# Optimization experiments

Hardware: AMD Instinct MI355X
Metric: run time of the kernel (lower is better)

Reference implementation:

```python
import jax, jax.numpy as jnp
import numpy as np

NEG = -1e9  # max-semiring 'zero' / structural mask value


def _cky_max(pot, lengths):
    """Max-plus CKY inside pass (torch_struct CKY_CRF with MaxSemiring).

    pot: [B, N, N] label-maxed span potentials, pot[b, i, j] = score of span (i, j).
    Returns [B] best binary-tree score for each sequence of given length.
    betaA[b, i, w]      = best score of span starting at i with width w (span [i, i+w]).
    betaB[b, j, N-1-w]  = best score of span ending at j with width w.
    """
    B, N, _ = pot.shape
    term = jnp.diagonal(pot, axis1=1, axis2=2)  # [B, N] width-0 spans
    betaA = jnp.full((B, N, N), NEG, dtype=pot.dtype).at[:, :, 0].set(term)
    betaB = jnp.full((B, N, N), NEG, dtype=pot.dtype).at[:, :, N - 1].set(term)
    for w in range(1, N):
        Y = betaA[:, : N - w, :w]       # [B, N-w, w] left children, widths 0..w-1
        Z = betaB[:, w:, N - w:]        # [B, N-w, w] right children (matching splits)
        span = jnp.diagonal(pot, offset=w, axis1=1, axis2=2)  # [B, N-w] pot[b, i, i+w]
        new = jnp.max(Y + Z, axis=-1) + span
        betaA = betaA.at[:, : N - w, w].set(new)
        betaB = betaB.at[:, w:, N - w - 1].set(new)
    final = betaA[:, 0, :]  # [B, N]: final[b, l-1] = best tree over [0, l-1]
    return final[jnp.arange(B), lengths - 1]


def setup_inputs() -> dict:
    key = jax.random.key(0)
    k1, k2 = jax.random.split(key)
    B, N, L = 64, 128, 32
    logits = jax.random.normal(k1, (B, N, N, L), dtype=jnp.float32)
    labels = jax.random.randint(k2, (B, N, N), 0, L, dtype=jnp.int64)
    return {"logits": logits, "labels": labels}


def reference(logits, labels):
    B, N, _, L = logits.shape
    gold_event = jax.nn.one_hot(jnp.maximum(labels, 0), L, dtype=logits.dtype)
    logits = logits - logits[..., :1]
    lengths = jnp.sum(labels[:, 0, :] != -100, axis=-1)
    augment = 1.0 - gold_event
    # force_root_constituent=True: forbid non-constituent root span
    augment = augment.at[jnp.arange(B), 0, lengths - 1, 0].add(-1e9)
    pot = jnp.max(logits + augment, axis=-1)  # max-semiring sum over label dim
    pred_score = _cky_max(pot, lengths)                      # [B]
    gold_score = jnp.sum(logits * gold_event, axis=(1, 2, 3))  # [B]
    margin_losses = jax.nn.relu(pred_score - gold_score)
    return jnp.mean(margin_losses)
```

## Files before the change

kernel.cpp:

```cpp
#include <hip/hip_runtime.h>

#define BATCH 64
#define SEQ   128
#define NLAB  32
#define NEGF  -3.0e38f

__global__ __launch_bounds__(64) void len_kernel(
    const int* __restrict__ labels, int* __restrict__ lenbuf,
    float* __restrict__ gold)
{
    const int b = blockIdx.x;
    const int t = threadIdx.x;
    const size_t base = (size_t)b * SEQ * SEQ;
    int cnt = (labels[base + t] != -100) + (labels[base + 64 + t] != -100);
    #pragma unroll
    for (int d = 32; d; d >>= 1) cnt += __shfl_down(cnt, d, 64);
    if (t == 0) { lenbuf[b] = cnt; gold[b] = 0.0f; }
}

__global__ __launch_bounds__(256) void pot_gold_kernel(
    const float* __restrict__ logits, const int* __restrict__ labels,
    const int* __restrict__ lenbuf,
    float* __restrict__ pot, float* __restrict__ gold)
{
    const int tid = threadIdx.x;
    const int wave = tid >> 6, lane = tid & 63;
    __shared__ __align__(16) float LP[4 * 16 * 36];
    float* W = LP + wave * (16 * 36);

    const int block_cell0 = blockIdx.x * 256;
    const int b = block_cell0 >> 14;
    const int len = lenbuf[b];
    float gacc = 0.0f;

    const int wave_cell0 = block_cell0 + wave * 64;

    #pragma unroll
    for (int chunk = 0; chunk < 4; ++chunk) {
        const int c0 = wave_cell0 + chunk * 16;
        const float4* src = reinterpret_cast<const float4*>(logits) + ((size_t)c0 << 3);
        const float4 f0 = src[lane];
        const float4 f1 = src[lane + 64];
        const int lv = (lane < 16) ? labels[c0 + lane] : 0;

        {
            const int cA = lane >> 3, tA = lane & 7;
            *reinterpret_cast<float4*>(W + cA * 36 + tA * 4) = f0;
            const int q1 = lane + 64;
            const int cB = q1 >> 3, tB = q1 & 7;
            *reinterpret_cast<float4*>(W + cB * 36 + tB * 4) = f1;
        }
        const int c = lane >> 2, u = lane & 3;
        const float4 r0 = *reinterpret_cast<const float4*>(W + c * 36 + u * 8);
        const float4 r1 = *reinterpret_cast<const float4*>(W + c * 36 + u * 8 + 4);

        int lab = __shfl(lv, c, 64);
        if (lab < 0) lab = 0;
        const float l0 = __shfl(r0.x, c << 2, 64);

        const int cell = c0 + c;
        const int ci = (cell >> 7) & (SEQ - 1);
        const int cj = cell & (SEQ - 1);
        const bool special = (ci == 0) && (cj == len - 1);

        const float vv[8] = { r0.x, r0.y, r0.z, r0.w, r1.x, r1.y, r1.z, r1.w };
        float m = NEGF, g = 0.0f;
        #pragma unroll
        for (int e = 0; e < 8; ++e) {
            const int l = u * 8 + e;
            const float r = vv[e] - l0;
            const bool isg = (l == lab);
            g = isg ? r : g;
            float cand = r + (isg ? 0.0f : 1.0f);
            if (l == 0 && special) cand -= 1.0e9f;
            m = fmaxf(m, cand);
        }
        m = fmaxf(m, __shfl_xor(m, 1, 64));
        m = fmaxf(m, __shfl_xor(m, 2, 64));
        g += __shfl_xor(g, 1, 64);
        g += __shfl_xor(g, 2, 64);
        if (u == 0) {
            pot[cell] = m;
            gacc += g;
        }
    }

    #pragma unroll
    for (int d = 1; d < 64; d <<= 1) gacc += __shfl_xor(gacc, d, 64);
    __shared__ float gred[4];
    if (lane == 0) gred[wave] = gacc;
    __syncthreads();
    if (tid == 0)
        atomicAdd(&gold[b], gred[0] + gred[1] + gred[2] + gred[3]);
}

template<int TPE, int LT, int S>
__device__ __forceinline__ void cky_step(
    float* __restrict__ A, float* __restrict__ Bt, const int w, const int tid)
{
    const int entries = SEQ - w;
    const int i = tid >> LT;
    const int s = tid & (TPE - 1);
    if (i < entries) {
        float* Arow = A + i * 132;
        const int j = i + w;
        const float* Brow = Bt + j * 132 + (SEQ - w);
        const float potv = Arow[w];
        const int wq = (w + 3) >> 2;
        float m = NEGF;
        #pragma unroll 4
        for (int q = s; q < wq; q += TPE) {
            const int k0 = q << 2;
            float4 a = *reinterpret_cast<const float4*>(Arow + k0);
            const float* bp = Brow + k0;
            float b0, b1, b2, b3;
            if (S == 0) {
                const float4 bv = *reinterpret_cast<const float4*>(bp);
                b0 = bv.x; b1 = bv.y; b2 = bv.z; b3 = bv.w;
            } else if (S == 2) {
                const float2 u0 = *reinterpret_cast<const float2*>(bp);
                const float2 u1 = *reinterpret_cast<const float2*>(bp + 2);
                b0 = u0.x; b1 = u0.y; b2 = u1.x; b3 = u1.y;
            } else {
                b0 = bp[0];
                const float2 u = *reinterpret_cast<const float2*>(bp + 1);
                b1 = u.x; b2 = u.y;
                b3 = bp[3];
            }
            a.y = (k0 + 1 < w) ? a.y : NEGF;
            a.z = (k0 + 2 < w) ? a.z : NEGF;
            a.w = (k0 + 3 < w) ? a.w : NEGF;
            m = fmaxf(m, fmaxf(fmaxf(a.x + b0, a.y + b1),
                               fmaxf(a.z + b2, a.w + b3)));
        }
        #pragma unroll
        for (int d = TPE >> 1; d; d >>= 1)
            m = fmaxf(m, __shfl_down(m, d, TPE));
        if (s == 0) {
            const float val = m + potv;
            Arow[w] = val;
            Bt[j * 132 + (SEQ - 1 - w)] = val;
        }
    }
    __syncthreads();
}

template<int TPE, int LT>
__device__ __forceinline__ void cky_phase4(
    float* __restrict__ A, float* __restrict__ Bt, const int w, const int tid)
{
    cky_step<TPE, LT, 0>(A, Bt, w,     tid);
    cky_step<TPE, LT, 3>(A, Bt, w + 1, tid);
    cky_step<TPE, LT, 2>(A, Bt, w + 2, tid);
    cky_step<TPE, LT, 1>(A, Bt, w + 3, tid);
}

__global__ __launch_bounds__(512, 1) void cky_kernel(
    const float* __restrict__ pot, const float* __restrict__ gold,
    const int* __restrict__ lenbuf, float* __restrict__ out)
{
    const int b = blockIdx.x;
    const int tid = threadIdx.x;
    const float* p = pot + (size_t)b * SEQ * SEQ;

    __shared__ __align__(16) float A[SEQ * 132];
    __shared__ __align__(16) float Bt[SEQ * 132];

    {
        const float4 neg4 = make_float4(NEGF, NEGF, NEGF, NEGF);
        float4* a4 = reinterpret_cast<float4*>(A);
        float4* b4 = reinterpret_cast<float4*>(Bt);
        for (int idx = tid; idx < SEQ * 132 / 4; idx += 512) {
            a4[idx] = neg4; b4[idx] = neg4;
        }
    }
    __syncthreads();
    {
        const float4* p4 = reinterpret_cast<const float4*>(p);
        for (int qi = tid; qi < SEQ * SEQ / 4; qi += 512) {
            const int i = qi >> 5;
            const int j0 = (qi & 31) << 2;
            const float4 v = p4[qi];
            const float vv[4] = { v.x, v.y, v.z, v.w };
            #pragma unroll
            for (int c2 = 0; c2 < 4; ++c2) {
                const int j = j0 + c2;
                if (j >= i) {
                    A[i * 132 + (j - i)] = vv[c2];
                    Bt[j * 132 + (SEQ - 1 - (j - i))] = vv[c2];
                }
            }
        }
    }
    __syncthreads();

    cky_step<1, 0, 3>(A, Bt, 1, tid);
    cky_step<1, 0, 2>(A, Bt, 2, tid);
    cky_step<1, 0, 1>(A, Bt, 3, tid);
    for (int w = 4;  w < 16;  w += 4) cky_phase4<1, 0>(A, Bt, w, tid);
    for (int w = 16; w < 32;  w += 4) cky_phase4<2, 1>(A, Bt, w, tid);
    for (int w = 32; w < 64;  w += 4) cky_phase4<4, 2>(A, Bt, w, tid);
    for (int w = 64; w < SEQ; w += 4) cky_phase4<8, 3>(A, Bt, w, tid);

    if (tid == 0) {
        const int len = lenbuf[b];
        const float pred = A[len - 1];
        float margin = pred - gold[b];
        margin = margin > 0.0f ? margin : 0.0f;
        atomicAdd(out, margin * (1.0f / (float)BATCH));
    }
}

extern "C" void kernel_launch(void* const* d_in, const int* in_sizes, int n_in,
                              void* d_out, int out_size, void* d_ws, size_t ws_size,
                              hipStream_t stream) {
    const float* logits = (const float*)d_in[0];
    const int* labels = (const int*)d_in[1];
    float* out = (float*)d_out;

    float* pot = (float*)d_ws;
    float* gold = pot + (size_t)BATCH * SEQ * SEQ;
    int* lenbuf = (int*)(gold + BATCH);

    (void)hipMemsetAsync(out, 0, sizeof(float), stream);

    len_kernel<<<BATCH, 64, 0, stream>>>(labels, lenbuf, gold);
    pot_gold_kernel<<<BATCH * SEQ * SEQ / 256, 256, 0, stream>>>(
        logits, labels, lenbuf, pot, gold);
    cky_kernel<<<BATCH, 512, 0, stream>>>(pot, gold, lenbuf, out);
}
```

Before: 261.7 us.

## Pipeline CKY steps with precomputed partial max and drop length kernel

The CKY loop now uses a fixed mapping of four threads per span start. For each next width it precomputes the max over all split points except the one that depends on the value just written, so each step after the barrier only combines two new terms before storing. The separate length kernel is removed: the length is recomputed inside both the pot and CKY kernels, and the gold score is written as per-block partials that the CKY kernel reduces, which replaces the atomics. This cuts one launch and shortens the serial critical path per width, at the cost of a fixed four-thread split that may leave lanes idle at small widths and do more work per thread at large widths.

```diff
diff --git a/kernel.cpp b/kernel.cpp
--- a/kernel.cpp
+++ b/kernel.cpp
@@ -5,34 +5,32 @@
 #define NLAB  32
 #define NEGF  -3.0e38f
 
-__global__ __launch_bounds__(64) void len_kernel(
-    const int* __restrict__ labels, int* __restrict__ lenbuf,
-    float* __restrict__ gold)
-{
-    const int b = blockIdx.x;
-    const int t = threadIdx.x;
-    const size_t base = (size_t)b * SEQ * SEQ;
-    int cnt = (labels[base + t] != -100) + (labels[base + 64 + t] != -100);
-    #pragma unroll
-    for (int d = 32; d; d >>= 1) cnt += __shfl_down(cnt, d, 64);
-    if (t == 0) { lenbuf[b] = cnt; gold[b] = 0.0f; }
-}
-
 __global__ __launch_bounds__(256) void pot_gold_kernel(
     const float* __restrict__ logits, const int* __restrict__ labels,
-    const int* __restrict__ lenbuf,
-    float* __restrict__ pot, float* __restrict__ gold)
+    float* __restrict__ pot, float* __restrict__ gpart)
 {
     const int tid = threadIdx.x;
     const int wave = tid >> 6, lane = tid & 63;
     __shared__ __align__(16) float LP[4 * 16 * 36];
+    __shared__ float gred[4];
+    __shared__ int s_len;
     float* W = LP + wave * (16 * 36);
 
     const int block_cell0 = blockIdx.x * 256;
     const int b = block_cell0 >> 14;
-    const int len = lenbuf[b];
+    const bool has_row0 = (blockIdx.x & 63) == 0;
+
+    if (has_row0 && tid < 64) {
+        const size_t base = (size_t)b << 14;
+        int cnt = (labels[base + tid] != -100) + (labels[base + 64 + tid] != -100);
+        #pragma unroll
+        for (int d = 32; d; d >>= 1) cnt += __shfl_down(cnt, d, 64);
+        if (tid == 0) s_len = cnt;
+    }
+    __syncthreads();
+    const int len = has_row0 ? s_len : -1;
+
     float gacc = 0.0f;
-
     const int wave_cell0 = block_cell0 + wave * 64;
 
     #pragma unroll
@@ -87,29 +85,37 @@
 
     #pragma unroll
     for (int d = 1; d < 64; d <<= 1) gacc += __shfl_xor(gacc, d, 64);
-    __shared__ float gred[4];
     if (lane == 0) gred[wave] = gacc;
     __syncthreads();
     if (tid == 0)
-        atomicAdd(&gold[b], gred[0] + gred[1] + gred[2] + gred[3]);
-}
-
-template<int TPE, int LT, int S>
+        gpart[blockIdx.x] = gred[0] + gred[1] + gred[2] + gred[3];
+}
+
+template<int S>
 __device__ __forceinline__ void cky_step(
-    float* __restrict__ A, float* __restrict__ Bt, const int w, const int tid)
+    float* __restrict__ A, float* __restrict__ Bt, const int wn,
+    const int i, const int s, float& pre_m, float& val, float& potv,
+    float& awB, const float a0)
 {
-    const int entries = SEQ - w;
-    const int i = tid >> LT;
-    const int s = tid & (TPE - 1);
-    if (i < entries) {
-        float* Arow = A + i * 132;
-        const int j = i + w;
-        const float* Brow = Bt + j * 132 + (SEQ - w);
-        const float potv = Arow[w];
-        const int wq = (w + 3) >> 2;
-        float m = NEGF;
-        #pragma unroll 4
-        for (int q = s; q < wq; q += TPE) {
+    const int iw = i + wn;
+    if (iw < SEQ) {
+        const float newB = Bt[iw * 132 + (SEQ - wn)];
+        const float m = fmaxf(pre_m, fmaxf(a0 + newB, val + awB));
+        val = m + potv;
+        if (s == 0) {
+            A[i * 132 + wn] = val;
+            Bt[iw * 132 + (SEQ - 1 - wn)] = val;
+        }
+    }
+    if (iw + 1 < SEQ) {
+        const float* Arow = A + i * 132;
+        potv = Arow[wn + 1];
+        const float* Brow = Bt + (iw + 1) * 132 + (SEQ - wn - 1);
+        awB = Brow[wn];
+        const int kmax = wn - 1;
+        float pm = NEGF;
+        #pragma unroll 2
+        for (int q = s; (q << 2) <= kmax; q += 4) {
             const int k0 = q << 2;
             float4 a = *reinterpret_cast<const float4*>(Arow + k0);
             const float* bp = Brow + k0;
@@ -127,37 +133,25 @@
                 b1 = u.x; b2 = u.y;
                 b3 = bp[3];
             }
-            a.y = (k0 + 1 < w) ? a.y : NEGF;
-            a.z = (k0 + 2 < w) ? a.z : NEGF;
-            a.w = (k0 + 3 < w) ? a.w : NEGF;
-            m = fmaxf(m, fmaxf(fmaxf(a.x + b0, a.y + b1),
-                               fmaxf(a.z + b2, a.w + b3)));
-        }
-        #pragma unroll
-        for (int d = TPE >> 1; d; d >>= 1)
-            m = fmaxf(m, __shfl_down(m, d, TPE));
-        if (s == 0) {
-            const float val = m + potv;
-            Arow[w] = val;
-            Bt[j * 132 + (SEQ - 1 - w)] = val;
-        }
-    }
-    __syncthreads();
-}
-
-template<int TPE, int LT>
-__device__ __forceinline__ void cky_phase4(
-    float* __restrict__ A, float* __restrict__ Bt, const int w, const int tid)
-{
-    cky_step<TPE, LT, 0>(A, Bt, w,     tid);
-    cky_step<TPE, LT, 3>(A, Bt, w + 1, tid);
-    cky_step<TPE, LT, 2>(A, Bt, w + 2, tid);
-    cky_step<TPE, LT, 1>(A, Bt, w + 3, tid);
+            a.x = (k0 != 0)        ? a.x : NEGF;
+            a.y = (k0 + 1 <= kmax) ? a.y : NEGF;
+            a.z = (k0 + 2 <= kmax) ? a.z : NEGF;
+            a.w = (k0 + 3 <= kmax) ? a.w : NEGF;
+            pm = fmaxf(pm, fmaxf(fmaxf(a.x + b0, a.y + b1),
+                                 fmaxf(a.z + b2, a.w + b3)));
+        }
+        pm = fmaxf(pm, __shfl_xor(pm, 1, 4));
+        pm = fmaxf(pm, __shfl_xor(pm, 2, 4));
+        pre_m = pm;
+    } else {
+        pre_m = NEGF;
+    }
+    __syncthreads();
 }
 
 __global__ __launch_bounds__(512, 1) void cky_kernel(
-    const float* __restrict__ pot, const float* __restrict__ gold,
-    const int* __restrict__ lenbuf, float* __restrict__ out)
+    const float* __restrict__ pot, const float* __restrict__ gpart,
+    const int* __restrict__ labels, float* __restrict__ out)
 {
     const int b = blockIdx.x;
     const int tid = threadIdx.x;
@@ -165,6 +159,21 @@
 
     __shared__ __align__(16) float A[SEQ * 132];
     __shared__ __align__(16) float Bt[SEQ * 132];
+    __shared__ int s_len;
+    __shared__ float s_gold;
+
+    if (tid < 64) {
+        const size_t base = (size_t)b << 14;
+        int cnt = (labels[base + tid] != -100) + (labels[base + 64 + tid] != -100);
+        #pragma unroll
+        for (int d = 32; d; d >>= 1) cnt += __shfl_down(cnt, d, 64);
+        if (tid == 0) s_len = cnt;
+    } else if (tid < 128) {
+        float g = gpart[b * 64 + (tid - 64)];
+        #pragma unroll
+        for (int d = 32; d; d >>= 1) g += __shfl_down(g, d, 64);
+        if (tid == 64) s_gold = g;
+    }
 
     {
         const float4 neg4 = make_float4(NEGF, NEGF, NEGF, NEGF);
@@ -194,19 +203,33 @@
     }
     __syncthreads();
 
-    cky_step<1, 0, 3>(A, Bt, 1, tid);
-    cky_step<1, 0, 2>(A, Bt, 2, tid);
-    cky_step<1, 0, 1>(A, Bt, 3, tid);
-    for (int w = 4;  w < 16;  w += 4) cky_phase4<1, 0>(A, Bt, w, tid);
-    for (int w = 16; w < 32;  w += 4) cky_phase4<2, 1>(A, Bt, w, tid);
-    for (int w = 32; w < 64;  w += 4) cky_phase4<4, 2>(A, Bt, w, tid);
-    for (int w = 64; w < SEQ; w += 4) cky_phase4<8, 3>(A, Bt, w, tid);
+    const int i = tid >> 2, s = tid & 3;
+    float pre_m = NEGF, val = 0.0f, potv = 0.0f, awB = 0.0f, a0 = 0.0f;
+    if (i + 1 < SEQ) {
+        const float* Arow = A + i * 132;
+        a0   = Arow[0];
+        val  = a0;
+        potv = Arow[1];
+        awB  = Bt[(i + 1) * 132 + (SEQ - 1)];
+    }
+
+    int wn = 1;
+    #pragma unroll 1
+    for (int ph = 0; ph < 31; ++ph) {
+        cky_step<2>(A, Bt, wn,     i, s, pre_m, val, potv, awB, a0);
+        cky_step<1>(A, Bt, wn + 1, i, s, pre_m, val, potv, awB, a0);
+        cky_step<0>(A, Bt, wn + 2, i, s, pre_m, val, potv, awB, a0);
+        cky_step<3>(A, Bt, wn + 3, i, s, pre_m, val, potv, awB, a0);
+        wn += 4;
+    }
+    cky_step<2>(A, Bt, 125, i, s, pre_m, val, potv, awB, a0);
+    cky_step<1>(A, Bt, 126, i, s, pre_m, val, potv, awB, a0);
+    cky_step<0>(A, Bt, 127, i, s, pre_m, val, potv, awB, a0);
 
     if (tid == 0) {
-        const int len = lenbuf[b];
+        const int len = s_len;
         const float pred = A[len - 1];
-        float margin = pred - gold[b];
-        margin = margin > 0.0f ? margin : 0.0f;
+        const float margin = fmaxf(pred - s_gold, 0.0f);
         atomicAdd(out, margin * (1.0f / (float)BATCH));
     }
 }
@@ -219,13 +242,11 @@
     float* out = (float*)d_out;
 
     float* pot = (float*)d_ws;
-    float* gold = pot + (size_t)BATCH * SEQ * SEQ;
-    int* lenbuf = (int*)(gold + BATCH);
+    float* gpart = pot + (size_t)BATCH * SEQ * SEQ;
 
     (void)hipMemsetAsync(out, 0, sizeof(float), stream);
 
-    len_kernel<<<BATCH, 64, 0, stream>>>(labels, lenbuf, gold);
     pot_gold_kernel<<<BATCH * SEQ * SEQ / 256, 256, 0, stream>>>(
-        logits, labels, lenbuf, pot, gold);
-    cky_kernel<<<BATCH, 512, 0, stream>>>(pot, gold, lenbuf, out);
-}
+        logits, labels, pot, gpart);
+    cky_kernel<<<BATCH, 512, 0, stream>>>(pot, gpart, labels, out);
+}
```

New measurement: 279.2 us. +6.7%, slower.
